# Kernel tuning notes

Hardware: AMD Instinct MI355X
Metric: run time of the kernel (lower is better)

## Reference

```python
import jax, jax.numpy as jnp
import numpy as np

H = 1024      # hidden_size
NH = 16       # attention heads
DH = H // NH  # head dim
B, S = 4, 2048
EPS = 1e-12


def setup_inputs() -> dict:
    key = jax.random.key(0)
    ks = jax.random.split(key, 9)
    sc = 1.0 / np.sqrt(H)
    inp = {
        "input_tensor": jax.random.normal(ks[0], (B, S, H), dtype=jnp.float32),
        "Wq": jax.random.normal(ks[1], (H, H), dtype=jnp.float32) * sc,
        "bq": jnp.zeros((H,), jnp.float32),
        "Wk": jax.random.normal(ks[2], (H, H), dtype=jnp.float32) * sc,
        "bk": jnp.zeros((H,), jnp.float32),
        "Wv": jax.random.normal(ks[3], (H, H), dtype=jnp.float32) * sc,
        "bv": jnp.zeros((H,), jnp.float32),
        "Wo": jax.random.normal(ks[4], (H, H), dtype=jnp.float32) * sc,
        "bo": jnp.zeros((H,), jnp.float32),
        "gamma": jnp.ones((H,), jnp.float32),
        "beta": jnp.zeros((H,), jnp.float32),
    }
    return inp


def _heads(x):
    # [B,S,H] -> [B,NH,S,DH]
    b, s, _ = x.shape
    return x.reshape(b, s, NH, DH).transpose(0, 2, 1, 3)


def reference(input_tensor, Wq, bq, Wk, bk, Wv, bv, Wo, bo, gamma, beta):
    q = _heads(input_tensor @ Wq.T + bq)
    k = _heads(input_tensor @ Wk.T + bk)
    v = _heads(input_tensor @ Wv.T + bv)
    scores = jnp.einsum("bhqd,bhkd->bhqk", q, k) / jnp.sqrt(jnp.float32(DH))
    probs = jax.nn.softmax(scores, axis=-1)  # dropout p=0 -> identity
    ctx = jnp.einsum("bhqk,bhkd->bhqd", probs, v)
    ctx = ctx.transpose(0, 2, 1, 3).reshape(input_tensor.shape)  # [B,S,H]
    h = ctx @ Wo.T + bo
    x = h + input_tensor
    u = jnp.mean(x, axis=-1, keepdims=True)
    s2 = jnp.mean((x - u) ** 2, axis=-1, keepdims=True)
    xn = (x - u) / jnp.sqrt(s2 + EPS)
    return gamma * xn + beta
```

## Files before the change

### kernel.cpp

```cpp
#include <hip/hip_runtime.h>
#include <math.h>

#define H   1024
#define NH  16
#define DH  64
#define BB  4
#define SS  2048
#define M_ROWS (BB*SS)
#define EPS 1e-12f
#define QSCALE 0.18033688011112042f

typedef __attribute__((ext_vector_type(4))) float f32x4;
typedef __attribute__((ext_vector_type(8))) short bf16x8;
typedef const __attribute__((address_space(1))) void* as1cvp;
typedef __attribute__((address_space(3))) void*       as3vp;

__device__ __forceinline__ unsigned short f2bf(float f) {
    union { float f; unsigned u; } x; x.f = f;
    unsigned r = x.u + 0x7fffu + ((x.u >> 16) & 1u);
    return (unsigned short)(r >> 16);
}
__device__ __forceinline__ unsigned pk2bf(float lo, float hi) {
    union { float f; unsigned u; } a, b; a.f = lo; b.f = hi;
    return (b.u & 0xffff0000u) | (a.u >> 16);
}

__global__ __launch_bounds__(256)
void cvt_all(const float4* __restrict__ x,
             const float4* __restrict__ wq, const float4* __restrict__ wk,
             const float4* __restrict__ wv, const float4* __restrict__ wo,
             ushort4* __restrict__ xb, ushort4* __restrict__ wqb,
             ushort4* __restrict__ wkb, ushort4* __restrict__ wvb,
             ushort4* __restrict__ wob)
{
    int id = blockIdx.x * 256 + threadIdx.x;
    const float4* src; ushort4* dst; int off;
    if (id < 2097152) { src = x; dst = xb; off = id; }
    else {
        int t = id - 2097152, wsel = t >> 18;
        off = t & 262143;
        src = wsel == 0 ? wq : wsel == 1 ? wk : wsel == 2 ? wv : wo;
        dst = wsel == 0 ? wqb : wsel == 1 ? wkb : wsel == 2 ? wvb : wob;
    }
    float4 v = src[off];
    ushort4 o; o.x = f2bf(v.x); o.y = f2bf(v.y); o.z = f2bf(v.z); o.w = f2bf(v.w);
    dst[off] = o;
}

__device__ __forceinline__ void gemm_core_128(const ushort* __restrict__ A,
                                              const ushort* __restrict__ Wt,
                                              ushort* AsP, ushort* BsP,
                                              int row0, int col0, int K,
                                              f32x4 (&acc)[4][4])
{
    const int tid = threadIdx.x, lane = tid & 63, w = tid >> 6;
    const int wr = w >> 1, wc = w & 1, l15 = lane & 15, quad = lane >> 4;
    const int lr = lane >> 2, kc = lane & 3;
    const int qs  = kc ^ ((lr >> 1) & 3);
    const int qsw = (quad ^ ((l15 >> 1) & 3)) * 8;

    const __attribute__((address_space(1))) ushort* gA =
        (const __attribute__((address_space(1))) ushort*)A;
    const __attribute__((address_space(1))) ushort* gB =
        (const __attribute__((address_space(1))) ushort*)Wt;
    __attribute__((address_space(3))) ushort* lA = (__attribute__((address_space(3))) ushort*)AsP;
    __attribute__((address_space(3))) ushort* lB = (__attribute__((address_space(3))) ushort*)BsP;

    const int ra = (w * 2) * 16 + lr;
    const int rb = ra + 16;

    for (int k0 = 0; k0 < K; k0 += 32) {
        __builtin_amdgcn_global_load_lds((as1cvp)(gA + (size_t)(row0 + ra) * K + k0 + qs * 8),
                                         (as3vp)(lA + (w * 2 + 0) * 512), 16, 0, 0);
        __builtin_amdgcn_global_load_lds((as1cvp)(gA + (size_t)(row0 + rb) * K + k0 + qs * 8),
                                         (as3vp)(lA + (w * 2 + 1) * 512), 16, 0, 0);
        __builtin_amdgcn_global_load_lds((as1cvp)(gB + (size_t)(col0 + ra) * K + k0 + qs * 8),
                                         (as3vp)(lB + (w * 2 + 0) * 512), 16, 0, 0);
        __builtin_amdgcn_global_load_lds((as1cvp)(gB + (size_t)(col0 + rb) * K + k0 + qs * 8),
                                         (as3vp)(lB + (w * 2 + 1) * 512), 16, 0, 0);
        __syncthreads();
        bf16x8 af[4], bfr[4];
        #pragma unroll
        for (int rt = 0; rt < 4; ++rt)
            af[rt] = *(const bf16x8*)&AsP[(wr * 64 + rt * 16 + l15) * 32 + qsw];
        #pragma unroll
        for (int ct = 0; ct < 4; ++ct)
            bfr[ct] = *(const bf16x8*)&BsP[(wc * 64 + ct * 16 + l15) * 32 + qsw];
        #pragma unroll
        for (int rt = 0; rt < 4; ++rt)
            #pragma unroll
            for (int ct = 0; ct < 4; ++ct)
                acc[rt][ct] = __builtin_amdgcn_mfma_f32_16x16x32_bf16(af[rt], bfr[ct], acc[rt][ct], 0, 0, 0);
        __syncthreads();
    }
}

__global__ __launch_bounds__(256)
void qkv_gemm(const ushort* __restrict__ xb,
              const ushort* __restrict__ Wqb, const ushort* __restrict__ Wkb,
              const ushort* __restrict__ Wvb,
              const float* __restrict__ bq, const float* __restrict__ bk,
              const float* __restrict__ bv,
              ushort* __restrict__ Qb, ushort* __restrict__ Kb, ushort* __restrict__ Vt)
{
    __shared__ ushort As[128 * 32];
    __shared__ ushort Bs[128 * 32];
    const int z = blockIdx.z;
    const ushort* Wt  = z == 0 ? Wqb : z == 1 ? Wkb : Wvb;
    const float* bias = z == 0 ? bq  : z == 1 ? bk  : bv;
    const int row0 = blockIdx.y * 128, col0 = blockIdx.x * 128;

    f32x4 acc[4][4];
    #pragma unroll
    for (int i = 0; i < 4; ++i)
        #pragma unroll
        for (int j = 0; j < 4; ++j)
            acc[i][j] = (f32x4){0.f, 0.f, 0.f, 0.f};

    gemm_core_128(xb, Wt, As, Bs, row0, col0, H, acc);

    const int tid = threadIdx.x, lane = tid & 63, w = tid >> 6;
    const int wr = w >> 1, wc = w & 1, l15 = lane & 15, quad = lane >> 4;

    #pragma unroll
    for (int rt = 0; rt < 4; ++rt) {
        const int r0g = row0 + wr * 64 + rt * 16 + quad * 4;
        #pragma unroll
        for (int ct = 0; ct < 4; ++ct) {
            const int c = col0 + wc * 64 + ct * 16 + l15;
            const float bs = bias[c];
            if (z == 0) {
                #pragma unroll
                for (int i = 0; i < 4; ++i)
                    Qb[(size_t)(r0g + i) * H + c] = f2bf((acc[rt][ct][i] + bs) * QSCALE);
            } else if (z == 1) {
                #pragma unroll
                for (int i = 0; i < 4; ++i)
                    Kb[(size_t)(r0g + i) * H + c] = f2bf(acc[rt][ct][i] + bs);
            } else {
                const int bb = r0g >> 11, s0 = r0g & 2047;
                const int hh = c >> 6, dd = c & 63;
                ushort4 o;
                o.x = f2bf(acc[rt][ct][0] + bs);
                o.y = f2bf(acc[rt][ct][1] + bs);
                o.z = f2bf(acc[rt][ct][2] + bs);
                o.w = f2bf(acc[rt][ct][3] + bs);
                *(ushort4*)&Vt[(((size_t)(bb * 16 + hh) * 64 + dd) << 11) + s0] = o;
            }
        }
    }
}

__global__ __launch_bounds__(256)
void oproj_gemm(const ushort* __restrict__ ctxb, const ushort* __restrict__ Wob,
                const float* __restrict__ bo, const float* __restrict__ res,
                float* __restrict__ Xr)
{
    __shared__ ushort As[128 * 32];
    __shared__ ushort Bs[128 * 32];
    const int row0 = blockIdx.y * 128, col0 = blockIdx.x * 128;

    f32x4 acc[4][4];
    #pragma unroll
    for (int i = 0; i < 4; ++i)
        #pragma unroll
        for (int j = 0; j < 4; ++j)
            acc[i][j] = (f32x4){0.f, 0.f, 0.f, 0.f};

    gemm_core_128(ctxb, Wob, As, Bs, row0, col0, H, acc);

    const int tid = threadIdx.x, lane = tid & 63, w = tid >> 6;
    const int wr = w >> 1, wc = w & 1, l15 = lane & 15, quad = lane >> 4;

    #pragma unroll
    for (int rt = 0; rt < 4; ++rt) {
        const int r0g = row0 + wr * 64 + rt * 16 + quad * 4;
        #pragma unroll
        for (int ct = 0; ct < 4; ++ct) {
            const int c = col0 + wc * 64 + ct * 16 + l15;
            const float bs = bo[c];
            #pragma unroll
            for (int i = 0; i < 4; ++i) {
                size_t idx = (size_t)(r0g + i) * H + c;
                Xr[idx] = acc[rt][ct][i] + bs + res[idx];
            }
        }
    }
}

#define KTILE 64
#define NKT (SS / KTILE)

__global__ __launch_bounds__(256, 4)
void flash_attn_mfma(const ushort* __restrict__ Qb, const ushort* __restrict__ Kb,
                     const ushort* __restrict__ Vt, ushort* __restrict__ ctx)
{
    __shared__ __align__(16) ushort Ks[2][KTILE * 64];
    __shared__ __align__(16) ushort Vs[2][64 * KTILE];
    __shared__ __align__(16) ushort Pw[4][16 * 64];

    const int tid  = threadIdx.x;
    const int lane = tid & 63;
    const int w    = tid >> 6;
    const int l15  = lane & 15, quad = lane >> 4;
    const int bh   = blockIdx.x & 63;
    const int qt   = blockIdx.x >> 6;
    const int b    = bh >> 4, h = bh & 15;
    const int row0 = qt * 64 + w * 16;
    const size_t qk_base = (size_t)(b * SS) * H + h * DH;
    const size_t vt_base = (size_t)((b * 16 + h) * 64) * SS;

    const __attribute__((address_space(1))) ushort* gK =
        (const __attribute__((address_space(1))) ushort*)Kb;
    const __attribute__((address_space(1))) ushort* gV =
        (const __attribute__((address_space(1))) ushort*)Vt;

    const int srow = lane >> 3;
    const int sck  = (lane & 7) ^ srow;

    const bf16x8 aq0 = *(const bf16x8*)&Qb[qk_base + (size_t)(row0 + l15) * H + quad * 8];
    const bf16x8 aq1 = *(const bf16x8*)&Qb[qk_base + (size_t)(row0 + l15) * H + 32 + quad * 8];

    float lp = 0.f;
    f32x4 o[4];
    #pragma unroll
    for (int dt = 0; dt < 4; ++dt) o[dt] = (f32x4){0.f, 0.f, 0.f, 0.f};

    #pragma unroll
    for (int t = 0; t < 2; ++t) {
        const int r = w * 16 + t * 8;
        __builtin_amdgcn_global_load_lds(
            (as1cvp)(gK + qk_base + (size_t)(r + srow) * H + sck * 8),
            (as3vp)(&Ks[0][r * 64]), 16, 0, 0);
        __builtin_amdgcn_global_load_lds(
            (as1cvp)(gV + vt_base + (size_t)(r + srow) * SS + sck * 8),
            (as3vp)(&Vs[0][r * 64]), 16, 0, 0);
    }

    unsigned* const P32 = (unsigned*)&Pw[w][0];
    const int prow = l15 * 32;
    const int psw  = l15 & 7;

    for (int kt = 0; kt < NKT; ++kt) {
        __syncthreads();

        if (kt + 1 < NKT) {
            const int j0 = (kt + 1) * KTILE;
            const int nb = (kt + 1) & 1;
            #pragma unroll
            for (int t = 0; t < 2; ++t) {
                const int r = w * 16 + t * 8;
                __builtin_amdgcn_global_load_lds(
                    (as1cvp)(gK + qk_base + (size_t)(j0 + r + srow) * H + sck * 8),
                    (as3vp)(&Ks[nb][r * 64]), 16, 0, 0);
                __builtin_amdgcn_global_load_lds(
                    (as1cvp)(gV + vt_base + (size_t)(r + srow) * SS + j0 + sck * 8),
                    (as3vp)(&Vs[nb][r * 64]), 16, 0, 0);
            }
        }

        const ushort* Ktile = Ks[kt & 1];
        const ushort* Vtile = Vs[kt & 1];

        f32x4 s[4];
        #pragma unroll
        for (int ct = 0; ct < 4; ++ct) {
            const int r = ct * 16 + l15;
            const bf16x8 k0 = *(const bf16x8*)&Ktile[r * 64 + ((quad ^ (r & 7)) * 8)];
            const bf16x8 k1 = *(const bf16x8*)&Ktile[r * 64 + (((4 | quad) ^ (r & 7)) * 8)];
            f32x4 z = (f32x4){0.f, 0.f, 0.f, 0.f};
            z = __builtin_amdgcn_mfma_f32_16x16x32_bf16(k0, aq0, z, 0, 0, 0);
            z = __builtin_amdgcn_mfma_f32_16x16x32_bf16(k1, aq1, z, 0, 0, 0);
            s[ct] = z;
        }

        #pragma unroll
        for (int ct = 0; ct < 4; ++ct) {
            const float p0 = __builtin_amdgcn_exp2f(fminf(s[ct][0], 115.f));
            const float p1 = __builtin_amdgcn_exp2f(fminf(s[ct][1], 115.f));
            const float p2 = __builtin_amdgcn_exp2f(fminf(s[ct][2], 115.f));
            const float p3 = __builtin_amdgcn_exp2f(fminf(s[ct][3], 115.f));
            lp += (p0 + p1) + (p2 + p3);
            uint2 pk;
            pk.x = pk2bf(p0, p1);
            pk.y = pk2bf(p2, p3);
            const int pc = ((ct * 2 + (quad >> 1)) ^ psw) * 4 + (quad & 1) * 2;
            *(uint2*)&P32[prow + pc] = pk;
        }

        const bf16x8 ap0 = *(const bf16x8*)&P32[prow + ((quad     ^ psw) * 4)];
        const bf16x8 ap1 = *(const bf16x8*)&P32[prow + (((4 | quad) ^ psw) * 4)];

        #pragma unroll
        for (int dt = 0; dt < 4; ++dt) {
            const int rv = dt * 16 + l15;
            const bf16x8 v0 = *(const bf16x8*)&Vtile[rv * 64 + ((quad ^ (rv & 7)) * 8)];
            const bf16x8 v1 = *(const bf16x8*)&Vtile[rv * 64 + (((4 | quad) ^ (rv & 7)) * 8)];
            o[dt] = __builtin_amdgcn_mfma_f32_16x16x32_bf16(ap0, v0, o[dt], 0, 0, 0);
            o[dt] = __builtin_amdgcn_mfma_f32_16x16x32_bf16(ap1, v1, o[dt], 0, 0, 0);
        }
    }

    float lr = lp;
    lr += __shfl_xor(lr, 16);
    lr += __shfl_xor(lr, 32);
    #pragma unroll
    for (int i = 0; i < 4; ++i) {
        const float inv = 1.f / __shfl(lr, quad * 4 + i);
        const int r = row0 + quad * 4 + i;
        #pragma unroll
        for (int dt = 0; dt < 4; ++dt)
            ctx[qk_base + (size_t)r * H + dt * 16 + l15] = f2bf(o[dt][i] * inv);
    }
}

__global__ __launch_bounds__(256)
void ln_kernel(const float* __restrict__ Xr, const float* __restrict__ gamma,
               const float* __restrict__ beta, float* __restrict__ out)
{
    __shared__ float red[256], red2[256];
    const int row = blockIdx.x;
    const int tid = threadIdx.x;
    const float4 v = ((const float4*)(Xr + (size_t)row * H))[tid];
    float s  = v.x + v.y + v.z + v.w;
    float ss = v.x * v.x + v.y * v.y + v.z * v.z + v.w * v.w;
    red[tid] = s; red2[tid] = ss;
    __syncthreads();
    for (int st = 128; st > 0; st >>= 1) {
        if (tid < st) { red[tid] += red[tid + st]; red2[tid] += red2[tid + st]; }
        __syncthreads();
    }
    const float mean = red[0] * (1.f / H);
    const float var  = red2[0] * (1.f / H) - mean * mean;
    const float rstd = rsqrtf(var + EPS);
    const float4 g  = ((const float4*)gamma)[tid];
    const float4 be = ((const float4*)beta)[tid];
    float4 o;
    o.x = g.x * (v.x - mean) * rstd + be.x;
    o.y = g.y * (v.y - mean) * rstd + be.y;
    o.z = g.z * (v.z - mean) * rstd + be.z;
    o.w = g.w * (v.w - mean) * rstd + be.w;
    ((float4*)(out + (size_t)row * H))[tid] = o;
}

extern "C" void kernel_launch(void* const* d_in, const int* in_sizes, int n_in,
                              void* d_out, int out_size, void* d_ws, size_t ws_size,
                              hipStream_t stream)
{
    const float* x     = (const float*)d_in[0];
    const float* Wq    = (const float*)d_in[1];
    const float* bq    = (const float*)d_in[2];
    const float* Wk    = (const float*)d_in[3];
    const float* bk    = (const float*)d_in[4];
    const float* Wv    = (const float*)d_in[5];
    const float* bv    = (const float*)d_in[6];
    const float* Wo    = (const float*)d_in[7];
    const float* bo    = (const float*)d_in[8];
    const float* gamma = (const float*)d_in[9];
    const float* beta  = (const float*)d_in[10];

    char* ws = (char*)d_ws;
    ushort* xb  = (ushort*)(ws);
    ushort* Wqb = (ushort*)(ws + (size_t)(16 << 20));
    ushort* Wkb = (ushort*)(ws + (size_t)(18 << 20));
    ushort* Wvb = (ushort*)(ws + (size_t)(20 << 20));
    ushort* Wob = (ushort*)(ws + (size_t)(22 << 20));
    ushort* Qb  = (ushort*)(ws + (size_t)(24 << 20));
    ushort* Kb  = (ushort*)(ws + (size_t)(40 << 20));
    ushort* Vt  = (ushort*)(ws + (size_t)(56 << 20));
    float*  Xr  = (float*) (ws + (size_t)(40 << 20));

    cvt_all<<<12288, 256, 0, stream>>>((const float4*)x, (const float4*)Wq, (const float4*)Wk,
                                       (const float4*)Wv, (const float4*)Wo,
                                       (ushort4*)xb, (ushort4*)Wqb, (ushort4*)Wkb,
                                       (ushort4*)Wvb, (ushort4*)Wob);

    qkv_gemm<<<dim3(H / 128, M_ROWS / 128, 3), 256, 0, stream>>>(
        xb, Wqb, Wkb, Wvb, bq, bk, bv, Qb, Kb, Vt);

    flash_attn_mfma<<<BB * NH * (SS / 64), 256, 0, stream>>>(Qb, Kb, Vt, Qb );

    oproj_gemm<<<dim3(H / 128, M_ROWS / 128), 256, 0, stream>>>(Qb, Wob, bo, x, Xr);

    ln_kernel<<<M_ROWS, 256, 0, stream>>>(Xr, gamma, beta, (float*)d_out);
}
```

Measured before the change: 324.3 us.

## Keep softmax probabilities in registers via permuted K rows, drop LDS P buffer

Permutes which K rows each QK MFMA lane group covers and changes the LDS swizzle, so the S output layout lines up with the A-operand layout of the PV MFMA. The P tile can then be packed straight from registers, which removes the per-tile LDS write and read of probabilities and its shared buffer. The change also precomputes LDS offsets, uses v_perm for bf16 packing, drops the exp clamp, adds s_setprio around the MFMA blocks and raises the occupancy hint to 5. Removing the clamp risks overflow if scores exceed the exp2 range, and the new permutation has to stay consistent with the swizzle.

```diff
diff --git a/kernel.cpp b/kernel.cpp
--- a/kernel.cpp
+++ b/kernel.cpp
@@ -21,8 +21,7 @@
     return (unsigned short)(r >> 16);
 }
 __device__ __forceinline__ unsigned pk2bf(float lo, float hi) {
-    union { float f; unsigned u; } a, b; a.f = lo; b.f = hi;
-    return (b.u & 0xffff0000u) | (a.u >> 16);
+    return __builtin_amdgcn_perm(__float_as_uint(hi), __float_as_uint(lo), 0x07060302u);
 }
 
 __global__ __launch_bounds__(256)
@@ -191,13 +190,12 @@
 #define KTILE 64
 #define NKT (SS / KTILE)
 
-__global__ __launch_bounds__(256, 4)
+__global__ __launch_bounds__(256, 5)
 void flash_attn_mfma(const ushort* __restrict__ Qb, const ushort* __restrict__ Kb,
                      const ushort* __restrict__ Vt, ushort* __restrict__ ctx)
 {
     __shared__ __align__(16) ushort Ks[2][KTILE * 64];
     __shared__ __align__(16) ushort Vs[2][64 * KTILE];
-    __shared__ __align__(16) ushort Pw[4][16 * 64];
 
     const int tid  = threadIdx.x;
     const int lane = tid & 63;
@@ -216,7 +214,26 @@
         (const __attribute__((address_space(1))) ushort*)Vt;
 
     const int srow = lane >> 3;
-    const int sck  = (lane & 7) ^ srow;
+    const int c8   = lane & 7;
+    const int sck0 = c8 ^ ((srow & 3) | (((w * 2 + 0) & 1) << 2));
+    const int sck1 = c8 ^ ((srow & 3) | (((w * 2 + 1) & 1) << 2));
+
+    const int fL = (l15 & 3) | (((l15 >> 2) & 1) << 2);
+    const int fV = (l15 & 3) | (((l15 >> 3) & 1) << 2);
+    const int rA = 8 * (l15 >> 2) + (l15 & 3);
+    int kOff0[4], kOff1[4], vOff0[4], vOff1[4];
+    #pragma unroll
+    for (int ct = 0; ct < 4; ++ct) {
+        const int r = rA + (ct & 1) * 4 + (ct >> 1) * 32;
+        kOff0[ct] = r * 64 + ((quad ^ fL) * 8);
+        kOff1[ct] = r * 64 + (((4 | quad) ^ fL) * 8);
+    }
+    #pragma unroll
+    for (int dt = 0; dt < 4; ++dt) {
+        const int rv = dt * 16 + l15;
+        vOff0[dt] = rv * 64 + ((quad ^ fV) * 8);
+        vOff1[dt] = rv * 64 + (((4 | quad) ^ fV) * 8);
+    }
 
     const bf16x8 aq0 = *(const bf16x8*)&Qb[qk_base + (size_t)(row0 + l15) * H + quad * 8];
     const bf16x8 aq1 = *(const bf16x8*)&Qb[qk_base + (size_t)(row0 + l15) * H + 32 + quad * 8];
@@ -226,20 +243,19 @@
     #pragma unroll
     for (int dt = 0; dt < 4; ++dt) o[dt] = (f32x4){0.f, 0.f, 0.f, 0.f};
 
-    #pragma unroll
-    for (int t = 0; t < 2; ++t) {
-        const int r = w * 16 + t * 8;
-        __builtin_amdgcn_global_load_lds(
-            (as1cvp)(gK + qk_base + (size_t)(r + srow) * H + sck * 8),
-            (as3vp)(&Ks[0][r * 64]), 16, 0, 0);
-        __builtin_amdgcn_global_load_lds(
-            (as1cvp)(gV + vt_base + (size_t)(r + srow) * SS + sck * 8),
-            (as3vp)(&Vs[0][r * 64]), 16, 0, 0);
-    }
-
-    unsigned* const P32 = (unsigned*)&Pw[w][0];
-    const int prow = l15 * 32;
-    const int psw  = l15 & 7;
+    const __attribute__((address_space(1))) ushort* gK0 =
+        gK + qk_base + (size_t)(w * 16 + srow) * H;
+    const __attribute__((address_space(1))) ushort* gV0 =
+        gV + vt_base + (size_t)(w * 16 + srow) * SS;
+
+    __builtin_amdgcn_global_load_lds((as1cvp)(gK0 + sck0 * 8),
+                                     (as3vp)(&Ks[0][(w * 16) * 64]), 16, 0, 0);
+    __builtin_amdgcn_global_load_lds((as1cvp)(gK0 + (size_t)8 * H + sck1 * 8),
+                                     (as3vp)(&Ks[0][(w * 16 + 8) * 64]), 16, 0, 0);
+    __builtin_amdgcn_global_load_lds((as1cvp)(gV0 + sck0 * 8),
+                                     (as3vp)(&Vs[0][(w * 16) * 64]), 16, 0, 0);
+    __builtin_amdgcn_global_load_lds((as1cvp)(gV0 + (size_t)8 * SS + sck1 * 8),
+                                     (as3vp)(&Vs[0][(w * 16 + 8) * 64]), 16, 0, 0);
 
     for (int kt = 0; kt < NKT; ++kt) {
         __syncthreads();
@@ -247,58 +263,56 @@
         if (kt + 1 < NKT) {
             const int j0 = (kt + 1) * KTILE;
             const int nb = (kt + 1) & 1;
-            #pragma unroll
-            for (int t = 0; t < 2; ++t) {
-                const int r = w * 16 + t * 8;
-                __builtin_amdgcn_global_load_lds(
-                    (as1cvp)(gK + qk_base + (size_t)(j0 + r + srow) * H + sck * 8),
-                    (as3vp)(&Ks[nb][r * 64]), 16, 0, 0);
-                __builtin_amdgcn_global_load_lds(
-                    (as1cvp)(gV + vt_base + (size_t)(r + srow) * SS + j0 + sck * 8),
-                    (as3vp)(&Vs[nb][r * 64]), 16, 0, 0);
-            }
+            __builtin_amdgcn_global_load_lds((as1cvp)(gK0 + (size_t)j0 * H + sck0 * 8),
+                                             (as3vp)(&Ks[nb][(w * 16) * 64]), 16, 0, 0);
+            __builtin_amdgcn_global_load_lds((as1cvp)(gK0 + (size_t)(j0 + 8) * H + sck1 * 8),
+                                             (as3vp)(&Ks[nb][(w * 16 + 8) * 64]), 16, 0, 0);
+            __builtin_amdgcn_global_load_lds((as1cvp)(gV0 + j0 + sck0 * 8),
+                                             (as3vp)(&Vs[nb][(w * 16) * 64]), 16, 0, 0);
+            __builtin_amdgcn_global_load_lds((as1cvp)(gV0 + (size_t)8 * SS + j0 + sck1 * 8),
+                                             (as3vp)(&Vs[nb][(w * 16 + 8) * 64]), 16, 0, 0);
         }
 
         const ushort* Ktile = Ks[kt & 1];
         const ushort* Vtile = Vs[kt & 1];
 
         f32x4 s[4];
+        __builtin_amdgcn_s_setprio(1);
         #pragma unroll
         for (int ct = 0; ct < 4; ++ct) {
-            const int r = ct * 16 + l15;
-            const bf16x8 k0 = *(const bf16x8*)&Ktile[r * 64 + ((quad ^ (r & 7)) * 8)];
-            const bf16x8 k1 = *(const bf16x8*)&Ktile[r * 64 + (((4 | quad) ^ (r & 7)) * 8)];
+            const bf16x8 k0 = *(const bf16x8*)&Ktile[kOff0[ct]];
+            const bf16x8 k1 = *(const bf16x8*)&Ktile[kOff1[ct]];
             f32x4 z = (f32x4){0.f, 0.f, 0.f, 0.f};
             z = __builtin_amdgcn_mfma_f32_16x16x32_bf16(k0, aq0, z, 0, 0, 0);
             z = __builtin_amdgcn_mfma_f32_16x16x32_bf16(k1, aq1, z, 0, 0, 0);
             s[ct] = z;
         }
-
+        __builtin_amdgcn_s_setprio(0);
+
+        unsigned pw[8];
         #pragma unroll
         for (int ct = 0; ct < 4; ++ct) {
-            const float p0 = __builtin_amdgcn_exp2f(fminf(s[ct][0], 115.f));
-            const float p1 = __builtin_amdgcn_exp2f(fminf(s[ct][1], 115.f));
-            const float p2 = __builtin_amdgcn_exp2f(fminf(s[ct][2], 115.f));
-            const float p3 = __builtin_amdgcn_exp2f(fminf(s[ct][3], 115.f));
+            const float p0 = __builtin_amdgcn_exp2f(s[ct][0]);
+            const float p1 = __builtin_amdgcn_exp2f(s[ct][1]);
+            const float p2 = __builtin_amdgcn_exp2f(s[ct][2]);
+            const float p3 = __builtin_amdgcn_exp2f(s[ct][3]);
             lp += (p0 + p1) + (p2 + p3);
-            uint2 pk;
-            pk.x = pk2bf(p0, p1);
-            pk.y = pk2bf(p2, p3);
-            const int pc = ((ct * 2 + (quad >> 1)) ^ psw) * 4 + (quad & 1) * 2;
-            *(uint2*)&P32[prow + pc] = pk;
-        }
-
-        const bf16x8 ap0 = *(const bf16x8*)&P32[prow + ((quad     ^ psw) * 4)];
-        const bf16x8 ap1 = *(const bf16x8*)&P32[prow + (((4 | quad) ^ psw) * 4)];
-
+            pw[ct * 2 + 0] = pk2bf(p0, p1);
+            pw[ct * 2 + 1] = pk2bf(p2, p3);
+        }
+        union { unsigned u[4]; bf16x8 v; } A0, A1;
+        A0.u[0] = pw[0]; A0.u[1] = pw[1]; A0.u[2] = pw[2]; A0.u[3] = pw[3];
+        A1.u[0] = pw[4]; A1.u[1] = pw[5]; A1.u[2] = pw[6]; A1.u[3] = pw[7];
+
+        __builtin_amdgcn_s_setprio(1);
         #pragma unroll
         for (int dt = 0; dt < 4; ++dt) {
-            const int rv = dt * 16 + l15;
-            const bf16x8 v0 = *(const bf16x8*)&Vtile[rv * 64 + ((quad ^ (rv & 7)) * 8)];
-            const bf16x8 v1 = *(const bf16x8*)&Vtile[rv * 64 + (((4 | quad) ^ (rv & 7)) * 8)];
-            o[dt] = __builtin_amdgcn_mfma_f32_16x16x32_bf16(ap0, v0, o[dt], 0, 0, 0);
-            o[dt] = __builtin_amdgcn_mfma_f32_16x16x32_bf16(ap1, v1, o[dt], 0, 0, 0);
-        }
+            const bf16x8 v0 = *(const bf16x8*)&Vtile[vOff0[dt]];
+            const bf16x8 v1 = *(const bf16x8*)&Vtile[vOff1[dt]];
+            o[dt] = __builtin_amdgcn_mfma_f32_16x16x32_bf16(A0.v, v0, o[dt], 0, 0, 0);
+            o[dt] = __builtin_amdgcn_mfma_f32_16x16x32_bf16(A1.v, v1, o[dt], 0, 0, 0);
+        }
+        __builtin_amdgcn_s_setprio(0);
     }
 
     float lr = lp;
```

After: 304.3 us. 6.2% less time.
